# Optimization experiments

Hardware: AMD Instinct MI355X
Metric: run time of the kernel (lower is better)

The kernel has to match this reference:

```python
import jax, jax.numpy as jnp
import numpy as np

DIM = 10
ITERATIONS = 2
N_NODES = 500_000
N_EDGES = 8_000_000


def _linear(x, W, b):
    # torch nn.Linear: y = x @ W.T + b
    return x @ W.T + b


def setup_inputs() -> dict:
    key = jax.random.key(0)
    ks = jax.random.split(key, 16)
    inp = {
        "h": jax.random.normal(ks[0], (N_NODES, DIM), dtype=jnp.float32),
        "edges": jax.random.randint(ks[1], (2, N_EDGES), 0, N_NODES, dtype=jnp.int64)
        if jax.config.jax_enable_x64
        else jax.random.randint(ks[1], (2, N_EDGES), 0, N_NODES, dtype=jnp.int32),
        "depth": jax.random.randint(ks[2], (N_NODES,), 0, 4, dtype=jnp.int32),
    }
    names = ["Wz", "bz", "Uz", "buz", "Wr", "br", "Ur", "bur", "Wh", "bh", "Uh", "buh"]
    s = 1.0 / np.sqrt(DIM)
    for i, n in enumerate(names):
        shape = (DIM, DIM) if n[0] in ("W", "U") else (DIM,)
        inp[n] = jax.random.uniform(ks[3 + i], shape, jnp.float32, -s, s)
    return inp


def reference(h, edges, depth, Wz, bz, Uz, buz, Wr, br, Ur, bur, Wh, bh, Uh, buh):
    recv, send = edges[0], edges[1]
    for i in range(ITERATIONS):
        active = (depth + i) <= ITERATIONS                      # [N] bool, shrinks with i
        h = jnp.where(active[:, None], h, 0.0)                  # drop inactive nodes (dict-key drop)
        # x[u] = sum over edges (u,v) with v active of h[v]; h already zeroed for inactive v
        x = jax.ops.segment_sum(h[send], recv, num_segments=h.shape[0])  # [N, DIM]
        z = jax.nn.sigmoid(_linear(x, Wz, bz) + _linear(h, Uz, buz))
        r = jax.nn.sigmoid(_linear(x, Wr, br) + _linear(h, Ur, bur))
        h_new = z * h + (1.0 - z) * jnp.tanh(_linear(x, Wh, bh) + _linear(r * h, Uh, buh))
        h = jnp.where(active[:, None], h_new, 0.0)
    return h
```

## Files before the change

kernel.cpp:

```cpp
#include <hip/hip_runtime.h>
#include <hip/hip_fp16.h>
#include <math.h>
#include <stdint.h>

#define DIM 10
#define NTILE 256
#define BKT_LOG 8
#define BKT 256
#define NBMAX 2048
#define EPW 2048
#define KPT (EPW / 256)
#define CAPB 2816
#define CAPF 1280
#define CAPK (CAPB - CAPF)
#define OVFCAP 32768
#define D2WORDS 32768


__device__ __forceinline__ float2 cvt2(uint32_t u) {
    __half2 hh = *reinterpret_cast<__half2*>(&u);
    return __half22float2(hh);
}

__device__ __forceinline__ int d2get(const uint32_t* __restrict__ depth2, int node) {
    uint32_t w = depth2[(uint32_t)node >> 4];
    return (int)((w >> ((node & 15) * 2)) & 3u);
}

__global__ void prep_kernel(const int* __restrict__ depth,
                            uint32_t* __restrict__ depth2,
                            uint32_t* __restrict__ cnts,
                            int n, int pack_blocks, int cnt_tot)
{
    __shared__ int sd[4096];
    const int t = threadIdx.x;
    const int bid = blockIdx.x;
    if (bid < pack_blocks) {
        const int base = bid * 4096;
        for (int i = t; i < 4096; i += 256) {
            int g = base + i;
            sd[i] = (g < n) ? depth[g] : 3;
        }
        __syncthreads();
        const int wbase = base >> 4;
        int wb = wbase + t;
        if (wb * 16 < n) {
            uint32_t v = 0;
            #pragma unroll
            for (int j = 0; j < 16; ++j)
                v |= ((uint32_t)(sd[t * 16 + j] & 3)) << (2 * j);
            depth2[wb] = v;
        }
    } else {
        int i = (bid - pack_blocks) * 256 + t;
        if (i < cnt_tot) cnts[i] = 0;
    }
}

__global__ __launch_bounds__(256) void binit_kernel(
                           const int* __restrict__ recv,
                           const int* __restrict__ send,
                           const uint32_t* __restrict__ depth2,
                           const int* __restrict__ depth,
                           const float* __restrict__ h_in,
                           uint16_t* __restrict__ h16a,
                           uint32_t* __restrict__ cntF,
                           uint32_t* __restrict__ cntB,
                           uint32_t* __restrict__ ovfc,
                           uint32_t* __restrict__ ovf,
                           uint32_t* __restrict__ bins,
                           int ne, int n, int bin_blocks)
{
    __shared__ uint32_t u[3 * NBMAX];
    const int t = threadIdx.x;
    const int bid = blockIdx.x;

    if (bid < bin_blocks) {
        uint32_t* lh  = u;
        uint32_t* wgF = u + NBMAX;
        uint32_t* wgB = u + 2 * NBMAX;
        for (int i = t; i < NBMAX; i += 256) lh[i] = 0;
        __syncthreads();

        const int base = bid * EPW;
        int rA[KPT], sA[KPT];
        #pragma unroll
        for (int k = 0; k < KPT; ++k) {
            int e = base + k * 256 + t;
            if (e < ne) { rA[k] = recv[e]; sA[k] = send[e]; }
            else        { rA[k] = -1;      sA[k] = 0;       }
        }
        int drA[KPT], dsA[KPT];
        #pragma unroll
        for (int k = 0; k < KPT; ++k) {
            if (rA[k] >= 0) { drA[k] = d2get(depth2, rA[k]); dsA[k] = d2get(depth2, sA[k]); }
            else            { drA[k] = 3;                    dsA[k] = 3;                    }
        }
        uint32_t fl = 0;
        #pragma unroll
        for (int k = 0; k < KPT; ++k) {
            if (rA[k] >= 0 && drA[k] <= 2 && dsA[k] <= 2) {
                bool f1 = (drA[k] <= 1) && (dsA[k] <= 1);
                fl |= (f1 ? 3u : 1u) << (2 * k);
                atomicAdd(&lh[rA[k] >> BKT_LOG], f1 ? 1u : 0x10000u);
            }
        }
        __syncthreads();

        for (int i = t; i < NBMAX; i += 256) {
            uint32_t v = lh[i];
            if (v) {
                uint32_t f = v & 0xffffu, kb = v >> 16;
                if (f)  wgF[i] = atomicAdd(&cntF[i], f);
                if (kb) wgB[i] = atomicAdd(&cntB[i], kb);
            }
        }
        __syncthreads();
        for (int i = t; i < NBMAX; i += 256) lh[i] = 0;
        __syncthreads();

        #pragma unroll
        for (int k = 0; k < KPT; ++k) {
            if ((fl >> (2 * k)) & 1u) {
                int r = rA[k], s = sA[k];
                int b = r >> BKT_LOG;
                bool f1 = (fl >> (2 * k)) & 2u;
                uint32_t w = (uint32_t)s | ((uint32_t)(r & (BKT - 1)) << 19)
                           | (f1 ? (1u << 27) : 0u);
                if (f1) {
                    uint32_t o = atomicAdd(&lh[b], 1u) & 0xffffu;
                    uint32_t pos = wgF[b] + o;
                    if (pos < CAPF) bins[(size_t)b * CAPB + pos] = w;
                    else { uint32_t oi = atomicAdd(ovfc, 1u);
                           if (oi < OVFCAP) ovf[oi] = (uint32_t)(base + k * 256 + t); }
                } else {
                    uint32_t o = atomicAdd(&lh[b], 0x10000u) >> 16;
                    uint32_t pos = wgB[b] + o;
                    if (pos < CAPK) bins[(size_t)b * CAPB + (CAPB - 1) - pos] = w;
                    else { uint32_t oi = atomicAdd(ovfc, 1u);
                           if (oi < OVFCAP) ovf[oi] = (uint32_t)(base + k * 256 + t); }
                }
            }
        }
    } else {
        float* sh = reinterpret_cast<float*>(u);
        const int tile = bid - bin_blocks;
        const int base = tile * NTILE;

        const long gbase = (long)base * DIM;
        const long glim  = (long)n * DIM;
        for (int idx = t; idx < NTILE * DIM; idx += NTILE) {
            long g = gbase + idx;
            float v = (g < glim) ? h_in[g] : 0.0f;
            sh[(idx / DIM) * 11 + (idx % DIM)] = v;
        }
        __syncthreads();

        const int node = base + t;
        if (node < n && depth[node] > 2) {
            #pragma unroll
            for (int c = 0; c < DIM; ++c) sh[t * 11 + c] = 0.0f;
        }
        __syncthreads();

        uint32_t* o16 = reinterpret_cast<uint32_t*>(h16a);
        const long o16base = (long)base * 8;
        const long o16lim  = (long)n * 8;
        for (int idx = t; idx < NTILE * 8; idx += NTILE) {
            long g = o16base + idx;
            if (g < o16lim) {
                int nl = idx / 8, c2 = idx % 8;
                uint32_t w = 0;
                if (c2 < 5) {
                    __half2 hh = __floats2half2_rn(sh[nl * 11 + 2 * c2],
                                                   sh[nl * 11 + 2 * c2 + 1]);
                    w = *reinterpret_cast<uint32_t*>(&hh);
                }
                o16[g] = w;
            }
        }
    }
}

template<int ITER>
__global__ __launch_bounds__(256) void scatgru_kernel(
                            const uint32_t* __restrict__ bins,
                            const uint32_t* __restrict__ cntF,
                            const uint32_t* __restrict__ cntB,
                            const uint32_t* __restrict__ ovfc,
                            const uint32_t* __restrict__ ovf,
                            const int* __restrict__ recv,
                            const int* __restrict__ send,
                            const int* __restrict__ depth,
                            const uint16_t* __restrict__ hcur,
                            uint16_t* __restrict__ hnext,
                            float* __restrict__ out32,
                            int n,
                            const float* __restrict__ Wz, const float* __restrict__ bz,
                            const float* __restrict__ Uz, const float* __restrict__ buz,
                            const float* __restrict__ Wr, const float* __restrict__ br,
                            const float* __restrict__ Ur, const float* __restrict__ bur,
                            const float* __restrict__ Wh, const float* __restrict__ bh,
                            const float* __restrict__ Uh, const float* __restrict__ buh)
{
    __shared__ float xl[BKT * DIM];
    __shared__ float sW[6][100];
    __shared__ float sb[3][10];

    const int t = threadIdx.x;
    if (t < 100) {
        sW[0][t] = Wz[t]; sW[1][t] = Uz[t];
        sW[2][t] = Wr[t]; sW[3][t] = Ur[t];
        sW[4][t] = Wh[t]; sW[5][t] = Uh[t];
    }
    if (t < 10) {
        sb[0][t] = bz[t] + buz[t];
        sb[1][t] = br[t] + bur[t];
        sb[2][t] = bh[t] + buh[t];
    }
    for (int i = t; i < BKT * DIM; i += 256) xl[i] = 0.0f;
    __syncthreads();

    const int b = blockIdx.x;
    const int n0 = b << BKT_LOG;
    const int nb = min(BKT, n - n0);

    const size_t base = (size_t)b * CAPB;
    const int fc = (int)min(cntF[b], (uint32_t)CAPF);
    int tot = fc, boff = 0;
    if (ITER == 0) {
        int bc = (int)min(cntB[b], (uint32_t)CAPK);
        tot = fc + bc;
        boff = CAPB - bc - fc;
    }

    for (int i0 = t; i0 < tot; i0 += 256 * 4) {
        uint32_t w[4];
        bool v[4];
        #pragma unroll
        for (int k = 0; k < 4; ++k) {
            int i = i0 + k * 256;
            v[k] = (i < tot);
            if (v[k]) {
                size_t idx = base + (size_t)((ITER == 0 && i >= fc) ? (i + boff) : i);
                w[k] = bins[idx];
            }
        }
        uint4 q[4]; uint32_t e8[4];
        #pragma unroll
        for (int k = 0; k < 4; ++k) {
            if (v[k]) {
                size_t s = (size_t)(w[k] & 0x7FFFFu);
                q[k]  = *reinterpret_cast<const uint4*>(hcur + s * 16);
                e8[k] = *reinterpret_cast<const uint32_t*>(hcur + s * 16 + 8);
            }
        }
        #pragma unroll
        for (int k = 0; k < 4; ++k) {
            if (v[k]) {
                float2 f0 = cvt2(q[k].x), f1 = cvt2(q[k].y);
                float2 f2 = cvt2(q[k].z), f3 = cvt2(q[k].w);
                float2 f4 = cvt2(e8[k]);
                float* xr = xl + ((w[k] >> 19) & (BKT - 1)) * DIM;
                atomicAdd(xr + 0, f0.x); atomicAdd(xr + 1, f0.y);
                atomicAdd(xr + 2, f1.x); atomicAdd(xr + 3, f1.y);
                atomicAdd(xr + 4, f2.x); atomicAdd(xr + 5, f2.y);
                atomicAdd(xr + 6, f3.x); atomicAdd(xr + 7, f3.y);
                atomicAdd(xr + 8, f4.x); atomicAdd(xr + 9, f4.y);
            }
        }
    }

    {
        const uint32_t cnt = min(*ovfc, (uint32_t)OVFCAP);
        for (uint32_t i = t; i < cnt; i += 256) {
            int e = (int)ovf[i];
            int r = recv[e];
            if ((r >> BKT_LOG) != b) continue;
            int s = send[e];
            if (ITER == 1 && (depth[r] > 1 || depth[s] > 1)) continue;
            uint4 q = *reinterpret_cast<const uint4*>(hcur + (size_t)s * 16);
            uint32_t e8v = *reinterpret_cast<const uint32_t*>(hcur + (size_t)s * 16 + 8);
            float2 f0 = cvt2(q.x), f1 = cvt2(q.y), f2 = cvt2(q.z), f3 = cvt2(q.w);
            float2 f4 = cvt2(e8v);
            float* xr = xl + (r & (BKT - 1)) * DIM;
            atomicAdd(xr + 0, f0.x); atomicAdd(xr + 1, f0.y);
            atomicAdd(xr + 2, f1.x); atomicAdd(xr + 3, f1.y);
            atomicAdd(xr + 4, f2.x); atomicAdd(xr + 5, f2.y);
            atomicAdd(xr + 6, f3.x); atomicAdd(xr + 7, f3.y);
            atomicAdd(xr + 8, f4.x); atomicAdd(xr + 9, f4.y);
        }
    }
    __syncthreads();

    if (t < nb) {
        const int node = n0 + t;
        const int dep = depth[node];
        const bool active = (dep + ITER) <= 2;

        float hv[DIM], xv[DIM], outv[DIM];
        {
            const uint16_t* hp = hcur + (size_t)node * 16;
            uint4 q = *reinterpret_cast<const uint4*>(hp);
            uint32_t e8v = *reinterpret_cast<const uint32_t*>(hp + 8);
            float2 f0 = cvt2(q.x), f1 = cvt2(q.y), f2 = cvt2(q.z), f3 = cvt2(q.w);
            float2 f4 = cvt2(e8v);
            hv[0] = f0.x; hv[1] = f0.y; hv[2] = f1.x; hv[3] = f1.y;
            hv[4] = f2.x; hv[5] = f2.y; hv[6] = f3.x; hv[7] = f3.y;
            hv[8] = f4.x; hv[9] = f4.y;
        }
        #pragma unroll
        for (int j = 0; j < DIM; ++j) xv[j] = xl[t * DIM + j];

        if (active) {
            float zz[DIM], rr[DIM];
            #pragma unroll
            for (int i = 0; i < DIM; ++i) {
                float az = sb[0][i];
                float ar = sb[1][i];
                #pragma unroll
                for (int j = 0; j < DIM; ++j) {
                    az = fmaf(xv[j], sW[0][i * DIM + j], az);
                    az = fmaf(hv[j], sW[1][i * DIM + j], az);
                    ar = fmaf(xv[j], sW[2][i * DIM + j], ar);
                    ar = fmaf(hv[j], sW[3][i * DIM + j], ar);
                }
                zz[i] = 1.0f / (1.0f + __expf(-az));
                rr[i] = 1.0f / (1.0f + __expf(-ar));
            }
            float rh[DIM];
            #pragma unroll
            for (int j = 0; j < DIM; ++j) rh[j] = rr[j] * hv[j];
            #pragma unroll
            for (int i = 0; i < DIM; ++i) {
                float ah = sb[2][i];
                #pragma unroll
                for (int j = 0; j < DIM; ++j) {
                    ah = fmaf(xv[j], sW[4][i * DIM + j], ah);
                    ah = fmaf(rh[j], sW[5][i * DIM + j], ah);
                }
                float th = tanhf(ah);
                outv[i] = zz[i] * hv[i] + (1.0f - zz[i]) * th;
            }
        } else {
            #pragma unroll
            for (int i = 0; i < DIM; ++i) outv[i] = hv[i];
        }

        if (ITER == 0) {
            if (dep > 1) {
                #pragma unroll
                for (int i = 0; i < DIM; ++i) outv[i] = 0.0f;
            }
            __half2 h01 = __floats2half2_rn(outv[0], outv[1]);
            __half2 h23 = __floats2half2_rn(outv[2], outv[3]);
            __half2 h45 = __floats2half2_rn(outv[4], outv[5]);
            __half2 h67 = __floats2half2_rn(outv[6], outv[7]);
            __half2 h89 = __floats2half2_rn(outv[8], outv[9]);
            uint4 o0;
            o0.x = *reinterpret_cast<uint32_t*>(&h01);
            o0.y = *reinterpret_cast<uint32_t*>(&h23);
            o0.z = *reinterpret_cast<uint32_t*>(&h45);
            o0.w = *reinterpret_cast<uint32_t*>(&h67);
            uint4 o1;
            o1.x = *reinterpret_cast<uint32_t*>(&h89);
            o1.y = 0; o1.z = 0; o1.w = 0;
            *reinterpret_cast<uint4*>(hnext + (size_t)node * 16)     = o0;
            *reinterpret_cast<uint4*>(hnext + (size_t)node * 16 + 8) = o1;
        } else {
            float2* op = reinterpret_cast<float2*>(out32 + (size_t)node * DIM);
            op[0] = make_float2(outv[0], outv[1]);
            op[1] = make_float2(outv[2], outv[3]);
            op[2] = make_float2(outv[4], outv[5]);
            op[3] = make_float2(outv[6], outv[7]);
            op[4] = make_float2(outv[8], outv[9]);
        }
    }
}

__global__ void init_mask32_kernel(const float* __restrict__ hsrc,
                                   float* __restrict__ hdst,
                                   const int* __restrict__ depth,
                                   int n)
{
    int node = blockIdx.x * blockDim.x + threadIdx.x;
    if (node >= n) return;
    bool act = depth[node] <= 2;
    const float* s = hsrc + (size_t)node * DIM;
    float* d = hdst + (size_t)node * DIM;
    #pragma unroll
    for (int c = 0; c < DIM; ++c) d[c] = act ? s[c] : 0.0f;
}

__global__ void simple_scatter_kernel(const int* __restrict__ recv,
                                      const int* __restrict__ send,
                                      const float* __restrict__ hm,
                                      float* __restrict__ x,
                                      int ne)
{
    const int tid = blockIdx.x * blockDim.x + threadIdx.x;
    const int e = tid / DIM;
    if (e >= ne) return;
    const int c = tid - e * DIM;
    const int s = send[e];
    const float v = hm[(size_t)s * DIM + c];
    if (v != 0.0f) {
        const int r = recv[e];
        unsafeAtomicAdd(x + (size_t)r * DIM + c, v);
    }
}

__global__ void zero_buf_kernel(float4* __restrict__ p, int tot4) {
    int i = blockIdx.x * blockDim.x + threadIdx.x;
    if (i < tot4) p[i] = make_float4(0.0f, 0.0f, 0.0f, 0.0f);
}

__global__ void gru32_kernel(const float* __restrict__ x,
                             const float* __restrict__ h,
                             float* __restrict__ out,
                             const int* __restrict__ depth, int iter, int n,
                             const float* __restrict__ Wz, const float* __restrict__ bz,
                             const float* __restrict__ Uz, const float* __restrict__ buz,
                             const float* __restrict__ Wr, const float* __restrict__ br,
                             const float* __restrict__ Ur, const float* __restrict__ bur,
                             const float* __restrict__ Wh, const float* __restrict__ bh,
                             const float* __restrict__ Uh, const float* __restrict__ buh)
{
    __shared__ float sW[6][100];
    __shared__ float sb[3][10];
    const int t = threadIdx.x;
    if (t < 100) {
        sW[0][t] = Wz[t]; sW[1][t] = Uz[t];
        sW[2][t] = Wr[t]; sW[3][t] = Ur[t];
        sW[4][t] = Wh[t]; sW[5][t] = Uh[t];
    }
    if (t < 10) {
        sb[0][t] = bz[t] + buz[t];
        sb[1][t] = br[t] + bur[t];
        sb[2][t] = bh[t] + buh[t];
    }
    __syncthreads();

    int node = blockIdx.x * blockDim.x + t;
    if (node >= n) return;
    const int dep = depth[node];
    const bool active = dep + iter <= 2;
    float xv[DIM], hv[DIM], outv[DIM];
    #pragma unroll
    for (int j = 0; j < DIM; ++j) {
        xv[j] = x[(size_t)node * DIM + j];
        hv[j] = h[(size_t)node * DIM + j];
    }
    if (active) {
        float zz[DIM], rr[DIM];
        #pragma unroll
        for (int i = 0; i < DIM; ++i) {
            float az = sb[0][i], ar = sb[1][i];
            #pragma unroll
            for (int j = 0; j < DIM; ++j) {
                az = fmaf(xv[j], sW[0][i * DIM + j], az);
                az = fmaf(hv[j], sW[1][i * DIM + j], az);
                ar = fmaf(xv[j], sW[2][i * DIM + j], ar);
                ar = fmaf(hv[j], sW[3][i * DIM + j], ar);
            }
            zz[i] = 1.0f / (1.0f + __expf(-az));
            rr[i] = 1.0f / (1.0f + __expf(-ar));
        }
        float rh[DIM];
        #pragma unroll
        for (int j = 0; j < DIM; ++j) rh[j] = rr[j] * hv[j];
        #pragma unroll
        for (int i = 0; i < DIM; ++i) {
            float ah = sb[2][i];
            #pragma unroll
            for (int j = 0; j < DIM; ++j) {
                ah = fmaf(xv[j], sW[4][i * DIM + j], ah);
                ah = fmaf(rh[j], sW[5][i * DIM + j], ah);
            }
            outv[i] = zz[i] * hv[i] + (1.0f - zz[i]) * tanhf(ah);
        }
    } else {
        #pragma unroll
        for (int i = 0; i < DIM; ++i) outv[i] = hv[i];
    }
    if (iter == 0 && dep > 1) {
        #pragma unroll
        for (int i = 0; i < DIM; ++i) outv[i] = 0.0f;
    }
    #pragma unroll
    for (int i = 0; i < DIM; ++i) out[(size_t)node * DIM + i] = outv[i];
}

extern "C" void kernel_launch(void* const* d_in, const int* in_sizes, int n_in,
                              void* d_out, int out_size, void* d_ws, size_t ws_size,
                              hipStream_t stream) {
    const float* h_in  = (const float*)d_in[0];
    const int*   edges = (const int*)d_in[1];
    const int*   depth = (const int*)d_in[2];
    const float* Wz  = (const float*)d_in[3];
    const float* bz  = (const float*)d_in[4];
    const float* Uz  = (const float*)d_in[5];
    const float* buz = (const float*)d_in[6];
    const float* Wr  = (const float*)d_in[7];
    const float* br  = (const float*)d_in[8];
    const float* Ur  = (const float*)d_in[9];
    const float* bur = (const float*)d_in[10];
    const float* Wh  = (const float*)d_in[11];
    const float* bh  = (const float*)d_in[12];
    const float* Uh  = (const float*)d_in[13];
    const float* buh = (const float*)d_in[14];

    const int n  = in_sizes[0] / DIM;
    const int ne = in_sizes[1] / 2;
    const int* recv = edges;
    const int* send = edges + ne;

    const int NB = (n + BKT - 1) >> BKT_LOG;
    const size_t meta_words = 2 * NBMAX + 8 + OVFCAP + D2WORDS;
    const size_t need = (size_t)n * 16 * sizeof(uint16_t) * 2
                      + (size_t)NB * CAPB * sizeof(uint32_t)
                      + meta_words * sizeof(uint32_t);

    const int BLK = 256;

    if (ws_size >= need && n <= (1 << 19) && NB <= NBMAX) {
        uint16_t* h16a = (uint16_t*)d_ws;
        uint16_t* h16b = h16a + (size_t)n * 16;
        uint32_t* bins = (uint32_t*)(h16b + (size_t)n * 16);
        uint32_t* meta = bins + (size_t)NB * CAPB;
        uint32_t* cntF   = meta;
        uint32_t* cntB   = meta + NBMAX;
        uint32_t* ovfc   = meta + 2 * NBMAX;
        uint32_t* ovf    = meta + 2 * NBMAX + 8;
        uint32_t* depth2 = meta + 2 * NBMAX + 8 + OVFCAP;

        const int bin_blocks  = (ne + EPW - 1) / EPW;
        const int node_blocks = (n + NTILE - 1) / NTILE;
        const int pack_blocks = (n + 4095) / 4096;
        const int cnt_tot = 2 * NBMAX + 1;
        const int cnt_blocks = (cnt_tot + 255) / 256;

        prep_kernel<<<pack_blocks + cnt_blocks, BLK, 0, stream>>>(
            depth, depth2, meta, n, pack_blocks, cnt_tot);
        binit_kernel<<<bin_blocks + node_blocks, BLK, 0, stream>>>(
            recv, send, depth2, depth, h_in, h16a,
            cntF, cntB, ovfc, ovf, bins, ne, n, bin_blocks);

        scatgru_kernel<0><<<NB, BLK, 0, stream>>>(
            bins, cntF, cntB, ovfc, ovf, recv, send, depth,
            h16a, h16b, nullptr, n,
            Wz, bz, Uz, buz, Wr, br, Ur, bur, Wh, bh, Uh, buh);

        scatgru_kernel<1><<<NB, BLK, 0, stream>>>(
            bins, cntF, cntB, ovfc, ovf, recv, send, depth,
            h16b, nullptr, (float*)d_out, n,
            Wz, bz, Uz, buz, Wr, br, Ur, bur, Wh, bh, Uh, buh);
    } else {
        float* x    = (float*)d_ws;
        float* hbuf = (float*)d_out;
        const int nwork = ne * DIM;
        const int edge_blocks = (nwork + BLK - 1) / BLK;
        const int x_tot4 = (n * DIM) / 4;
        const int xz_blocks = (x_tot4 + BLK - 1) / BLK;
        const int nb2 = (n + BLK - 1) / BLK;

        init_mask32_kernel<<<nb2, BLK, 0, stream>>>(h_in, hbuf, depth, n);
        zero_buf_kernel<<<xz_blocks, BLK, 0, stream>>>((float4*)x, x_tot4);
        simple_scatter_kernel<<<edge_blocks, BLK, 0, stream>>>(recv, send, hbuf, x, ne);
        gru32_kernel<<<nb2, BLK, 0, stream>>>(x, hbuf, hbuf, depth, 0, n,
            Wz, bz, Uz, buz, Wr, br, Ur, bur, Wh, bh, Uh, buh);
        zero_buf_kernel<<<xz_blocks, BLK, 0, stream>>>((float4*)x, x_tot4);
        simple_scatter_kernel<<<edge_blocks, BLK, 0, stream>>>(recv, send, hbuf, x, ne);
        gru32_kernel<<<nb2, BLK, 0, stream>>>(x, hbuf, hbuf, depth, 1, n,
            Wz, bz, Uz, buz, Wr, br, Ur, bur, Wh, bh, Uh, buh);
    }
}
```

Measured before the change: 646.7 us.

## Partition edge bins by sender range and split scatter from GRU

Edge binning now uses a 2D grid of cells indexed by sender partition (s>>16) and receiver bucket, filled by direct global atomics instead of a block-local histogram with reservation. Scatter runs one block per cell, so each block's gathers from h touch a narrower sender range. Each block accumulates into shared memory, then atomically adds to an fp32 x buffer placed in the output. Overflow edges are handled by a separate kernel, and the GRU becomes its own per-node kernel that also re-zeros x. The trade-off is more global atomics and kernel launches, plus iteration-1 scans that no longer skip non-frontier bins cheaply.

```diff
diff --git a/kernel.cpp b/kernel.cpp
--- a/kernel.cpp
+++ b/kernel.cpp
@@ -10,11 +10,12 @@
 #define NBMAX 2048
 #define EPW 2048
 #define KPT (EPW / 256)
-#define CAPB 2816
-#define CAPF 1280
-#define CAPK (CAPB - CAPF)
+#define NPART 8
+#define PSHIFT 16
+#define CAP 448
 #define OVFCAP 32768
 #define D2WORDS 32768
+#define XSTR 11
 
 
 __device__ __forceinline__ float2 cvt2(uint32_t u) {
@@ -30,7 +31,9 @@
 __global__ void prep_kernel(const int* __restrict__ depth,
                             uint32_t* __restrict__ depth2,
                             uint32_t* __restrict__ cnts,
-                            int n, int pack_blocks, int cnt_tot)
+                            float4* __restrict__ x4,
+                            int n, int pack_blocks, int cnt_tot, int cnt_blocks,
+                            int x_tot4)
 {
     __shared__ int sd[4096];
     const int t = threadIdx.x;
@@ -42,8 +45,7 @@
             sd[i] = (g < n) ? depth[g] : 3;
         }
         __syncthreads();
-        const int wbase = base >> 4;
-        int wb = wbase + t;
+        int wb = (base >> 4) + t;
         if (wb * 16 < n) {
             uint32_t v = 0;
             #pragma unroll
@@ -51,9 +53,12 @@
                 v |= ((uint32_t)(sd[t * 16 + j] & 3)) << (2 * j);
             depth2[wb] = v;
         }
-    } else {
+    } else if (bid < pack_blocks + cnt_blocks) {
         int i = (bid - pack_blocks) * 256 + t;
         if (i < cnt_tot) cnts[i] = 0;
+    } else {
+        int i = (bid - pack_blocks - cnt_blocks) * 256 + t;
+        if (i < x_tot4) x4[i] = make_float4(0.0f, 0.0f, 0.0f, 0.0f);
     }
 }
 
@@ -64,24 +69,17 @@
                            const int* __restrict__ depth,
                            const float* __restrict__ h_in,
                            uint16_t* __restrict__ h16a,
-                           uint32_t* __restrict__ cntF,
-                           uint32_t* __restrict__ cntB,
+                           uint32_t* __restrict__ cnt,
                            uint32_t* __restrict__ ovfc,
                            uint32_t* __restrict__ ovf,
                            uint32_t* __restrict__ bins,
-                           int ne, int n, int bin_blocks)
-{
-    __shared__ uint32_t u[3 * NBMAX];
+                           int ne, int n, int NB, int bin_blocks)
+{
+    __shared__ float sh[NTILE * 11];
     const int t = threadIdx.x;
     const int bid = blockIdx.x;
 
     if (bid < bin_blocks) {
-        uint32_t* lh  = u;
-        uint32_t* wgF = u + NBMAX;
-        uint32_t* wgB = u + 2 * NBMAX;
-        for (int i = t; i < NBMAX; i += 256) lh[i] = 0;
-        __syncthreads();
-
         const int base = bid * EPW;
         int rA[KPT], sA[KPT];
         #pragma unroll
@@ -96,57 +94,22 @@
             if (rA[k] >= 0) { drA[k] = d2get(depth2, rA[k]); dsA[k] = d2get(depth2, sA[k]); }
             else            { drA[k] = 3;                    dsA[k] = 3;                    }
         }
-        uint32_t fl = 0;
         #pragma unroll
         for (int k = 0; k < KPT; ++k) {
             if (rA[k] >= 0 && drA[k] <= 2 && dsA[k] <= 2) {
+                int r = rA[k], s = sA[k];
                 bool f1 = (drA[k] <= 1) && (dsA[k] <= 1);
-                fl |= (f1 ? 3u : 1u) << (2 * k);
-                atomicAdd(&lh[rA[k] >> BKT_LOG], f1 ? 1u : 0x10000u);
-            }
-        }
-        __syncthreads();
-
-        for (int i = t; i < NBMAX; i += 256) {
-            uint32_t v = lh[i];
-            if (v) {
-                uint32_t f = v & 0xffffu, kb = v >> 16;
-                if (f)  wgF[i] = atomicAdd(&cntF[i], f);
-                if (kb) wgB[i] = atomicAdd(&cntB[i], kb);
-            }
-        }
-        __syncthreads();
-        for (int i = t; i < NBMAX; i += 256) lh[i] = 0;
-        __syncthreads();
-
-        #pragma unroll
-        for (int k = 0; k < KPT; ++k) {
-            if ((fl >> (2 * k)) & 1u) {
-                int r = rA[k], s = sA[k];
-                int b = r >> BKT_LOG;
-                bool f1 = (fl >> (2 * k)) & 2u;
                 uint32_t w = (uint32_t)s | ((uint32_t)(r & (BKT - 1)) << 19)
                            | (f1 ? (1u << 27) : 0u);
-                if (f1) {
-                    uint32_t o = atomicAdd(&lh[b], 1u) & 0xffffu;
-                    uint32_t pos = wgF[b] + o;
-                    if (pos < CAPF) bins[(size_t)b * CAPB + pos] = w;
-                    else { uint32_t oi = atomicAdd(ovfc, 1u);
-                           if (oi < OVFCAP) ovf[oi] = (uint32_t)(base + k * 256 + t); }
-                } else {
-                    uint32_t o = atomicAdd(&lh[b], 0x10000u) >> 16;
-                    uint32_t pos = wgB[b] + o;
-                    if (pos < CAPK) bins[(size_t)b * CAPB + (CAPB - 1) - pos] = w;
-                    else { uint32_t oi = atomicAdd(ovfc, 1u);
-                           if (oi < OVFCAP) ovf[oi] = (uint32_t)(base + k * 256 + t); }
-                }
+                int cell = (s >> PSHIFT) * NB + (r >> BKT_LOG);
+                uint32_t pos = atomicAdd(&cnt[cell], 1u);
+                if (pos < CAP) bins[(size_t)cell * CAP + pos] = w;
+                else { uint32_t oi = atomicAdd(ovfc, 1u);
+                       if (oi < OVFCAP) ovf[oi] = (uint32_t)(base + k * 256 + t); }
             }
         }
     } else {
-        float* sh = reinterpret_cast<float*>(u);
-        const int tile = bid - bin_blocks;
-        const int base = tile * NTILE;
-
+        const int base = (bid - bin_blocks) * NTILE;
         const long gbase = (long)base * DIM;
         const long glim  = (long)n * DIM;
         for (int idx = t; idx < NTILE * DIM; idx += NTILE) {
@@ -155,14 +118,12 @@
             sh[(idx / DIM) * 11 + (idx % DIM)] = v;
         }
         __syncthreads();
-
         const int node = base + t;
         if (node < n && depth[node] > 2) {
             #pragma unroll
             for (int c = 0; c < DIM; ++c) sh[t * 11 + c] = 0.0f;
         }
         __syncthreads();
-
         uint32_t* o16 = reinterpret_cast<uint32_t*>(h16a);
         const long o16base = (long)base * 8;
         const long o16lim  = (long)n * 8;
@@ -183,30 +144,93 @@
 }
 
 template<int ITER>
-__global__ __launch_bounds__(256) void scatgru_kernel(
+__global__ __launch_bounds__(256) void scat_kernel(
                             const uint32_t* __restrict__ bins,
-                            const uint32_t* __restrict__ cntF,
-                            const uint32_t* __restrict__ cntB,
-                            const uint32_t* __restrict__ ovfc,
-                            const uint32_t* __restrict__ ovf,
-                            const int* __restrict__ recv,
-                            const int* __restrict__ send,
-                            const int* __restrict__ depth,
-                            const uint16_t* __restrict__ hcur,
-                            uint16_t* __restrict__ hnext,
-                            float* __restrict__ out32,
-                            int n,
-                            const float* __restrict__ Wz, const float* __restrict__ bz,
-                            const float* __restrict__ Uz, const float* __restrict__ buz,
-                            const float* __restrict__ Wr, const float* __restrict__ br,
-                            const float* __restrict__ Ur, const float* __restrict__ bur,
-                            const float* __restrict__ Wh, const float* __restrict__ bh,
-                            const float* __restrict__ Uh, const float* __restrict__ buh)
-{
-    __shared__ float xl[BKT * DIM];
+                            const uint32_t* __restrict__ cnt,
+                            const uint16_t* __restrict__ h16,
+                            float* __restrict__ x,
+                            int n, int NB)
+{
+    __shared__ float xl[BKT * XSTR];
+    const int t = threadIdx.x;
+    const int cellid = blockIdx.x;
+    const int b = cellid % NB;
+    const int n0 = b << BKT_LOG;
+    const int nb = min(BKT, n - n0);
+
+    for (int i = t; i < BKT * XSTR; i += 256) xl[i] = 0.0f;
+    __syncthreads();
+
+    const size_t base = (size_t)cellid * CAP;
+    const int tot = (int)min(cnt[cellid], (uint32_t)CAP);
+
+    for (int i = t; i < tot; i += 256) {
+        uint32_t w = bins[base + i];
+        if (ITER == 1 && !((w >> 27) & 1u)) continue;
+        size_t s = (size_t)(w & 0x7FFFFu);
+        uint4 q = *reinterpret_cast<const uint4*>(h16 + s * 16);
+        uint32_t e8 = *reinterpret_cast<const uint32_t*>(h16 + s * 16 + 8);
+        float2 f0 = cvt2(q.x), f1 = cvt2(q.y), f2 = cvt2(q.z), f3 = cvt2(q.w);
+        float2 f4 = cvt2(e8);
+        float* xr = xl + ((w >> 19) & (BKT - 1)) * XSTR;
+        atomicAdd(xr + 0, f0.x); atomicAdd(xr + 1, f0.y);
+        atomicAdd(xr + 2, f1.x); atomicAdd(xr + 3, f1.y);
+        atomicAdd(xr + 4, f2.x); atomicAdd(xr + 5, f2.y);
+        atomicAdd(xr + 6, f3.x); atomicAdd(xr + 7, f3.y);
+        atomicAdd(xr + 8, f4.x); atomicAdd(xr + 9, f4.y);
+    }
+    __syncthreads();
+
+    float* xo = x + (size_t)n0 * DIM;
+    for (int i = t; i < nb * DIM; i += 256) {
+        float v = xl[(i / DIM) * XSTR + (i % DIM)];
+        if (v != 0.0f) unsafeAtomicAdd(xo + i, v);
+    }
+}
+
+__global__ void ovf_apply_kernel(const uint32_t* __restrict__ ovfc,
+                                 const uint32_t* __restrict__ ovf,
+                                 const int* __restrict__ recv,
+                                 const int* __restrict__ send,
+                                 const int* __restrict__ depth,
+                                 const uint16_t* __restrict__ h16,
+                                 float* __restrict__ x,
+                                 int iter)
+{
+    const uint32_t cntv = min(*ovfc, (uint32_t)OVFCAP);
+    for (uint32_t i = blockIdx.x * blockDim.x + threadIdx.x; i < cntv;
+         i += gridDim.x * blockDim.x) {
+        int e = (int)ovf[i];
+        int r = recv[e], s = send[e];
+        if (iter == 1 && (depth[r] > 1 || depth[s] > 1)) continue;
+        uint4 q = *reinterpret_cast<const uint4*>(h16 + (size_t)s * 16);
+        uint32_t e8 = *reinterpret_cast<const uint32_t*>(h16 + (size_t)s * 16 + 8);
+        float2 f0 = cvt2(q.x), f1 = cvt2(q.y), f2 = cvt2(q.z), f3 = cvt2(q.w);
+        float2 f4 = cvt2(e8);
+        float* xr = x + (size_t)r * DIM;
+        unsafeAtomicAdd(xr + 0, f0.x); unsafeAtomicAdd(xr + 1, f0.y);
+        unsafeAtomicAdd(xr + 2, f1.x); unsafeAtomicAdd(xr + 3, f1.y);
+        unsafeAtomicAdd(xr + 4, f2.x); unsafeAtomicAdd(xr + 5, f2.y);
+        unsafeAtomicAdd(xr + 6, f3.x); unsafeAtomicAdd(xr + 7, f3.y);
+        unsafeAtomicAdd(xr + 8, f4.x); unsafeAtomicAdd(xr + 9, f4.y);
+    }
+}
+
+template<int LAST>
+__global__ __launch_bounds__(256) void gru_kernel(
+                           float* xio,
+                           const uint16_t* __restrict__ hcur,
+                           uint16_t* __restrict__ hnext,
+                           const int* __restrict__ depth, int n,
+                           const float* __restrict__ Wz, const float* __restrict__ bz,
+                           const float* __restrict__ Uz, const float* __restrict__ buz,
+                           const float* __restrict__ Wr, const float* __restrict__ br,
+                           const float* __restrict__ Ur, const float* __restrict__ bur,
+                           const float* __restrict__ Wh, const float* __restrict__ bh,
+                           const float* __restrict__ Uh, const float* __restrict__ buh)
+{
     __shared__ float sW[6][100];
     __shared__ float sb[3][10];
-
     const int t = threadIdx.x;
     if (t < 100) {
         sW[0][t] = Wz[t]; sW[1][t] = Uz[t];
@@ -218,170 +242,91 @@
         sb[1][t] = br[t] + bur[t];
         sb[2][t] = bh[t] + buh[t];
     }
-    for (int i = t; i < BKT * DIM; i += 256) xl[i] = 0.0f;
     __syncthreads();
 
-    const int b = blockIdx.x;
-    const int n0 = b << BKT_LOG;
-    const int nb = min(BKT, n - n0);
-
-    const size_t base = (size_t)b * CAPB;
-    const int fc = (int)min(cntF[b], (uint32_t)CAPF);
-    int tot = fc, boff = 0;
-    if (ITER == 0) {
-        int bc = (int)min(cntB[b], (uint32_t)CAPK);
-        tot = fc + bc;
-        boff = CAPB - bc - fc;
-    }
-
-    for (int i0 = t; i0 < tot; i0 += 256 * 4) {
-        uint32_t w[4];
-        bool v[4];
-        #pragma unroll
-        for (int k = 0; k < 4; ++k) {
-            int i = i0 + k * 256;
-            v[k] = (i < tot);
-            if (v[k]) {
-                size_t idx = base + (size_t)((ITER == 0 && i >= fc) ? (i + boff) : i);
-                w[k] = bins[idx];
+    const int node = blockIdx.x * 256 + t;
+    if (node >= n) return;
+    const int dep = depth[node];
+    const int iter = LAST ? 1 : 0;
+    const bool active = (dep + iter) <= 2;
+
+    float hv[DIM];
+    {
+        const uint16_t* hp = hcur + (size_t)node * 16;
+        uint4 q = *reinterpret_cast<const uint4*>(hp);
+        uint32_t e8 = *reinterpret_cast<const uint32_t*>(hp + 8);
+        float2 f0 = cvt2(q.x), f1 = cvt2(q.y), f2 = cvt2(q.z), f3 = cvt2(q.w);
+        float2 f4 = cvt2(e8);
+        hv[0] = f0.x; hv[1] = f0.y; hv[2] = f1.x; hv[3] = f1.y;
+        hv[4] = f2.x; hv[5] = f2.y; hv[6] = f3.x; hv[7] = f3.y;
+        hv[8] = f4.x; hv[9] = f4.y;
+    }
+    float xv[DIM];
+    #pragma unroll
+    for (int j = 0; j < DIM; ++j) xv[j] = xio[(size_t)node * DIM + j];
+
+    float outv[DIM];
+    if (active) {
+        float zz[DIM], rh[DIM];
+        #pragma unroll
+        for (int i = 0; i < DIM; ++i) {
+            float az = sb[0][i], ar = sb[1][i];
+            #pragma unroll
+            for (int j = 0; j < DIM; ++j) {
+                az = fmaf(xv[j], sW[0][i * DIM + j], az);
+                az = fmaf(hv[j], sW[1][i * DIM + j], az);
+                ar = fmaf(xv[j], sW[2][i * DIM + j], ar);
+                ar = fmaf(hv[j], sW[3][i * DIM + j], ar);
             }
-        }
-        uint4 q[4]; uint32_t e8[4];
-        #pragma unroll
-        for (int k = 0; k < 4; ++k) {
-            if (v[k]) {
-                size_t s = (size_t)(w[k] & 0x7FFFFu);
-                q[k]  = *reinterpret_cast<const uint4*>(hcur + s * 16);
-                e8[k] = *reinterpret_cast<const uint32_t*>(hcur + s * 16 + 8);
+            zz[i] = 1.0f / (1.0f + __expf(-az));
+            rh[i] = (1.0f / (1.0f + __expf(-ar))) * hv[i];
+        }
+        #pragma unroll
+        for (int i = 0; i < DIM; ++i) {
+            float ah = sb[2][i];
+            #pragma unroll
+            for (int j = 0; j < DIM; ++j) {
+                ah = fmaf(xv[j], sW[4][i * DIM + j], ah);
+                ah = fmaf(rh[j], sW[5][i * DIM + j], ah);
             }
-        }
-        #pragma unroll
-        for (int k = 0; k < 4; ++k) {
-            if (v[k]) {
-                float2 f0 = cvt2(q[k].x), f1 = cvt2(q[k].y);
-                float2 f2 = cvt2(q[k].z), f3 = cvt2(q[k].w);
-                float2 f4 = cvt2(e8[k]);
-                float* xr = xl + ((w[k] >> 19) & (BKT - 1)) * DIM;
-                atomicAdd(xr + 0, f0.x); atomicAdd(xr + 1, f0.y);
-                atomicAdd(xr + 2, f1.x); atomicAdd(xr + 3, f1.y);
-                atomicAdd(xr + 4, f2.x); atomicAdd(xr + 5, f2.y);
-                atomicAdd(xr + 6, f3.x); atomicAdd(xr + 7, f3.y);
-                atomicAdd(xr + 8, f4.x); atomicAdd(xr + 9, f4.y);
-            }
-        }
-    }
-
-    {
-        const uint32_t cnt = min(*ovfc, (uint32_t)OVFCAP);
-        for (uint32_t i = t; i < cnt; i += 256) {
-            int e = (int)ovf[i];
-            int r = recv[e];
-            if ((r >> BKT_LOG) != b) continue;
-            int s = send[e];
-            if (ITER == 1 && (depth[r] > 1 || depth[s] > 1)) continue;
-            uint4 q = *reinterpret_cast<const uint4*>(hcur + (size_t)s * 16);
-            uint32_t e8v = *reinterpret_cast<const uint32_t*>(hcur + (size_t)s * 16 + 8);
-            float2 f0 = cvt2(q.x), f1 = cvt2(q.y), f2 = cvt2(q.z), f3 = cvt2(q.w);
-            float2 f4 = cvt2(e8v);
-            float* xr = xl + (r & (BKT - 1)) * DIM;
-            atomicAdd(xr + 0, f0.x); atomicAdd(xr + 1, f0.y);
-            atomicAdd(xr + 2, f1.x); atomicAdd(xr + 3, f1.y);
-            atomicAdd(xr + 4, f2.x); atomicAdd(xr + 5, f2.y);
-            atomicAdd(xr + 6, f3.x); atomicAdd(xr + 7, f3.y);
-            atomicAdd(xr + 8, f4.x); atomicAdd(xr + 9, f4.y);
-        }
-    }
-    __syncthreads();
-
-    if (t < nb) {
-        const int node = n0 + t;
-        const int dep = depth[node];
-        const bool active = (dep + ITER) <= 2;
-
-        float hv[DIM], xv[DIM], outv[DIM];
-        {
-            const uint16_t* hp = hcur + (size_t)node * 16;
-            uint4 q = *reinterpret_cast<const uint4*>(hp);
-            uint32_t e8v = *reinterpret_cast<const uint32_t*>(hp + 8);
-            float2 f0 = cvt2(q.x), f1 = cvt2(q.y), f2 = cvt2(q.z), f3 = cvt2(q.w);
-            float2 f4 = cvt2(e8v);
-            hv[0] = f0.x; hv[1] = f0.y; hv[2] = f1.x; hv[3] = f1.y;
-            hv[4] = f2.x; hv[5] = f2.y; hv[6] = f3.x; hv[7] = f3.y;
-            hv[8] = f4.x; hv[9] = f4.y;
-        }
-        #pragma unroll
-        for (int j = 0; j < DIM; ++j) xv[j] = xl[t * DIM + j];
-
-        if (active) {
-            float zz[DIM], rr[DIM];
-            #pragma unroll
-            for (int i = 0; i < DIM; ++i) {
-                float az = sb[0][i];
-                float ar = sb[1][i];
-                #pragma unroll
-                for (int j = 0; j < DIM; ++j) {
-                    az = fmaf(xv[j], sW[0][i * DIM + j], az);
-                    az = fmaf(hv[j], sW[1][i * DIM + j], az);
-                    ar = fmaf(xv[j], sW[2][i * DIM + j], ar);
-                    ar = fmaf(hv[j], sW[3][i * DIM + j], ar);
-                }
-                zz[i] = 1.0f / (1.0f + __expf(-az));
-                rr[i] = 1.0f / (1.0f + __expf(-ar));
-            }
-            float rh[DIM];
-            #pragma unroll
-            for (int j = 0; j < DIM; ++j) rh[j] = rr[j] * hv[j];
-            #pragma unroll
-            for (int i = 0; i < DIM; ++i) {
-                float ah = sb[2][i];
-                #pragma unroll
-                for (int j = 0; j < DIM; ++j) {
-                    ah = fmaf(xv[j], sW[4][i * DIM + j], ah);
-                    ah = fmaf(rh[j], sW[5][i * DIM + j], ah);
-                }
-                float th = tanhf(ah);
-                outv[i] = zz[i] * hv[i] + (1.0f - zz[i]) * th;
-            }
-        } else {
-            #pragma unroll
-            for (int i = 0; i < DIM; ++i) outv[i] = hv[i];
-        }
-
-        if (ITER == 0) {
-            if (dep > 1) {
-                #pragma unroll
-                for (int i = 0; i < DIM; ++i) outv[i] = 0.0f;
-            }
-            __half2 h01 = __floats2half2_rn(outv[0], outv[1]);
-            __half2 h23 = __floats2half2_rn(outv[2], outv[3]);
-            __half2 h45 = __floats2half2_rn(outv[4], outv[5]);
-            __half2 h67 = __floats2half2_rn(outv[6], outv[7]);
-            __half2 h89 = __floats2half2_rn(outv[8], outv[9]);
-            uint4 o0;
-            o0.x = *reinterpret_cast<uint32_t*>(&h01);
-            o0.y = *reinterpret_cast<uint32_t*>(&h23);
-            o0.z = *reinterpret_cast<uint32_t*>(&h45);
-            o0.w = *reinterpret_cast<uint32_t*>(&h67);
-            uint4 o1;
-            o1.x = *reinterpret_cast<uint32_t*>(&h89);
-            o1.y = 0; o1.z = 0; o1.w = 0;
-            *reinterpret_cast<uint4*>(hnext + (size_t)node * 16)     = o0;
-            *reinterpret_cast<uint4*>(hnext + (size_t)node * 16 + 8) = o1;
-        } else {
-            float2* op = reinterpret_cast<float2*>(out32 + (size_t)node * DIM);
-            op[0] = make_float2(outv[0], outv[1]);
-            op[1] = make_float2(outv[2], outv[3]);
-            op[2] = make_float2(outv[4], outv[5]);
-            op[3] = make_float2(outv[6], outv[7]);
-            op[4] = make_float2(outv[8], outv[9]);
-        }
+            outv[i] = zz[i] * hv[i] + (1.0f - zz[i]) * tanhf(ah);
+        }
+    } else {
+        #pragma unroll
+        for (int i = 0; i < DIM; ++i) outv[i] = hv[i];
+    }
+
+    if (!LAST) {
+        if (dep > 1) {
+            #pragma unroll
+            for (int i = 0; i < DIM; ++i) outv[i] = 0.0f;
+        }
+        __half2 h01 = __floats2half2_rn(outv[0], outv[1]);
+        __half2 h23 = __floats2half2_rn(outv[2], outv[3]);
+        __half2 h45 = __floats2half2_rn(outv[4], outv[5]);
+        __half2 h67 = __floats2half2_rn(outv[6], outv[7]);
+        __half2 h89 = __floats2half2_rn(outv[8], outv[9]);
+        uint4 o0;
+        o0.x = *reinterpret_cast<uint32_t*>(&h01);
+        o0.y = *reinterpret_cast<uint32_t*>(&h23);
+        o0.z = *reinterpret_cast<uint32_t*>(&h45);
+        o0.w = *reinterpret_cast<uint32_t*>(&h67);
+        uint4 o1;
+        o1.x = *reinterpret_cast<uint32_t*>(&h89);
+        o1.y = 0; o1.z = 0; o1.w = 0;
+        *reinterpret_cast<uint4*>(hnext + (size_t)node * 16)     = o0;
+        *reinterpret_cast<uint4*>(hnext + (size_t)node * 16 + 8) = o1;
+        #pragma unroll
+        for (int j = 0; j < DIM; ++j) xio[(size_t)node * DIM + j] = 0.0f;
+    } else {
+        #pragma unroll
+        for (int j = 0; j < DIM; ++j) xio[(size_t)node * DIM + j] = outv[j];
     }
 }
 
 __global__ void init_mask32_kernel(const float* __restrict__ hsrc,
                                    float* __restrict__ hdst,
-                                   const int* __restrict__ depth,
-                                   int n)
+                                   const int* __restrict__ depth, int n)
 {
     int node = blockIdx.x * blockDim.x + threadIdx.x;
     if (node >= n) return;
@@ -395,8 +340,7 @@
 __global__ void simple_scatter_kernel(const int* __restrict__ recv,
                                       const int* __restrict__ send,
                                       const float* __restrict__ hm,
-                                      float* __restrict__ x,
-                                      int ne)
+                                      float* __restrict__ x, int ne)
 {
     const int tid = blockIdx.x * blockDim.x + threadIdx.x;
     const int e = tid / DIM;
@@ -452,7 +396,7 @@
         hv[j] = h[(size_t)node * DIM + j];
     }
     if (active) {
-        float zz[DIM], rr[DIM];
+        float zz[DIM], rh[DIM];
         #pragma unroll
         for (int i = 0; i < DIM; ++i) {
             float az = sb[0][i], ar = sb[1][i];
@@ -464,11 +408,8 @@
                 ar = fmaf(hv[j], sW[3][i * DIM + j], ar);
             }
             zz[i] = 1.0f / (1.0f + __expf(-az));
-            rr[i] = 1.0f / (1.0f + __expf(-ar));
-        }
-        float rh[DIM];
-        #pragma unroll
-        for (int j = 0; j < DIM; ++j) rh[j] = rr[j] * hv[j];
+            rh[i] = (1.0f / (1.0f + __expf(-ar))) * hv[i];
+        }
         #pragma unroll
         for (int i = 0; i < DIM; ++i) {
             float ah = sb[2][i];
@@ -516,44 +457,46 @@
     const int* send = edges + ne;
 
     const int NB = (n + BKT - 1) >> BKT_LOG;
-    const size_t meta_words = 2 * NBMAX + 8 + OVFCAP + D2WORDS;
+    const size_t meta_words = (size_t)NPART * NBMAX + 8 + OVFCAP + D2WORDS;
     const size_t need = (size_t)n * 16 * sizeof(uint16_t) * 2
-                      + (size_t)NB * CAPB * sizeof(uint32_t)
+                      + (size_t)NPART * NB * CAP * sizeof(uint32_t)
                       + meta_words * sizeof(uint32_t);
 
     const int BLK = 256;
 
-    if (ws_size >= need && n <= (1 << 19) && NB <= NBMAX) {
+    if (ws_size >= need && n <= (1 << 19) && NB <= NBMAX && out_size >= n * DIM) {
         uint16_t* h16a = (uint16_t*)d_ws;
         uint16_t* h16b = h16a + (size_t)n * 16;
         uint32_t* bins = (uint32_t*)(h16b + (size_t)n * 16);
-        uint32_t* meta = bins + (size_t)NB * CAPB;
-        uint32_t* cntF   = meta;
-        uint32_t* cntB   = meta + NBMAX;
-        uint32_t* ovfc   = meta + 2 * NBMAX;
-        uint32_t* ovf    = meta + 2 * NBMAX + 8;
-        uint32_t* depth2 = meta + 2 * NBMAX + 8 + OVFCAP;
+        uint32_t* meta = bins + (size_t)NPART * NB * CAP;
+        uint32_t* cnt    = meta;
+        uint32_t* ovfc   = meta + (size_t)NPART * NBMAX;
+        uint32_t* ovf    = ovfc + 8;
+        uint32_t* depth2 = ovf + OVFCAP;
+        float*    x      = (float*)d_out;
 
         const int bin_blocks  = (ne + EPW - 1) / EPW;
         const int node_blocks = (n + NTILE - 1) / NTILE;
         const int pack_blocks = (n + 4095) / 4096;
-        const int cnt_tot = 2 * NBMAX + 1;
+        const int cnt_tot = NPART * NBMAX + 1;
         const int cnt_blocks = (cnt_tot + 255) / 256;
-
-        prep_kernel<<<pack_blocks + cnt_blocks, BLK, 0, stream>>>(
-            depth, depth2, meta, n, pack_blocks, cnt_tot);
+        const int x_tot4 = n * DIM / 4;
+        const int x_blocks = (x_tot4 + 255) / 256;
+
+        prep_kernel<<<pack_blocks + cnt_blocks + x_blocks, BLK, 0, stream>>>(
+            depth, depth2, cnt, (float4*)x, n, pack_blocks, cnt_tot, cnt_blocks, x_tot4);
         binit_kernel<<<bin_blocks + node_blocks, BLK, 0, stream>>>(
             recv, send, depth2, depth, h_in, h16a,
-            cntF, cntB, ovfc, ovf, bins, ne, n, bin_blocks);
-
-        scatgru_kernel<0><<<NB, BLK, 0, stream>>>(
-            bins, cntF, cntB, ovfc, ovf, recv, send, depth,
-            h16a, h16b, nullptr, n,
+            cnt, ovfc, ovf, bins, ne, n, NB, bin_blocks);
+
+        scat_kernel<0><<<NPART * NB, BLK, 0, stream>>>(bins, cnt, h16a, x, n, NB);
+        ovf_apply_kernel<<<16, BLK, 0, stream>>>(ovfc, ovf, recv, send, depth, h16a, x, 0);
+        gru_kernel<0><<<node_blocks, BLK, 0, stream>>>(x, h16a, h16b, depth, n,
             Wz, bz, Uz, buz, Wr, br, Ur, bur, Wh, bh, Uh, buh);
 
-        scatgru_kernel<1><<<NB, BLK, 0, stream>>>(
-            bins, cntF, cntB, ovfc, ovf, recv, send, depth,
-            h16b, nullptr, (float*)d_out, n,
+        scat_kernel<1><<<NPART * NB, BLK, 0, stream>>>(bins, cnt, h16b, x, n, NB);
+        ovf_apply_kernel<<<16, BLK, 0, stream>>>(ovfc, ovf, recv, send, depth, h16b, x, 1);
+        gru_kernel<1><<<node_blocks, BLK, 0, stream>>>(x, h16b, nullptr, depth, n,
             Wz, bz, Uz, buz, Wr, br, Ur, bur, Wh, bh, Uh, buh);
     } else {
         float* x    = (float*)d_ws;
```

After: 696.8 us. 7.8% more time.
